# Optimization experiments

Measured on AMD Instinct MI355X. Metric: run time of the kernel, lower is better.

The kernel has to match this reference:

```python
import jax, jax.numpy as jnp
import numpy as np

B, T, D = 32, 4096, 64
K = 512
COMMITMENT_COST = 0.25


def setup_inputs() -> dict:
    key = jax.random.key(0)
    kz, kw = jax.random.split(key)
    z = jax.random.normal(kz, (B, T, D), dtype=jnp.float32)
    # matches nn.init.uniform_(weight, -1/K, 1/K)
    W = jax.random.uniform(kw, (K, D), dtype=jnp.float32, minval=-1.0 / K, maxval=1.0 / K)
    return {"z": z, "W": W}


def reference(z, W):
    b, t, d = z.shape
    z_flat = z.reshape(-1, d)                                   # [N, D]
    # squared euclidean distances via ||z||^2 + ||w||^2 - 2 z.w
    dist = (jnp.sum(z_flat * z_flat, axis=1, keepdims=True)
            + jnp.sum(W * W, axis=1)
            - 2.0 * z_flat @ W.T)                               # [N, K]
    indices = jnp.argmin(dist, axis=1)                          # [N]
    z_q = W[indices].reshape(b, t, d)                           # gather
    # straight-through estimator
    z_q_st = z + jax.lax.stop_gradient(z_q - z)
    loss = COMMITMENT_COST * jnp.mean((z - jax.lax.stop_gradient(z_q_st)) ** 2)
    return z_q_st, indices.reshape(b, t), loss
```

## Files before the change

### kernel.cpp

```cpp
#include <hip/hip_runtime.h>
#include <hip/hip_bf16.h>
#include <math.h>

#define NROWS 131072
#define KC    512
#define DD    64
#define NELEM (NROWS * DD)

#define OUT_IDX_OFF  NELEM
#define OUT_LOSS_OFF (NELEM + NROWS)

#define MARGIN 3e-5f

#define WSO_CNT   0
#define WSO_DONE  4
#define WSO_LOSS  8
#define WSO_WNORM 64
#define WSO_BH    4096
#define WSO_BL    (WSO_BH + 65536)
#define WSO_LIST  (WSO_BL + 65536)

typedef __attribute__((ext_vector_type(8))) short short8;
typedef __attribute__((ext_vector_type(4))) float f32x4;

__device__ __forceinline__ short f2bf_bits(float f) {
  __hip_bfloat16 h = __float2bfloat16(f);
  short s; __builtin_memcpy(&s, &h, 2); return s;
}
__device__ __forceinline__ float bfbits2f(short s) {
  __hip_bfloat16 h; __builtin_memcpy(&h, &s, 2);
  return __bfloat162float(h);
}
__device__ __forceinline__ void cvt8(const float* __restrict__ p, short8& hi, short8& lo) {
#pragma unroll
  for (int j = 0; j < 8; j++) {
    float f = p[j];
    short hb = f2bf_bits(f);
    float r = f - bfbits2f(hb);
    hi[j] = hb;
    lo[j] = f2bf_bits(r);
  }
}

__device__ __forceinline__ float np_sumsq64(const float* __restrict__ p) {
#pragma clang fp contract(off)
  float r0 = p[0] * p[0], r1 = p[1] * p[1], r2 = p[2] * p[2], r3 = p[3] * p[3];
  float r4 = p[4] * p[4], r5 = p[5] * p[5], r6 = p[6] * p[6], r7 = p[7] * p[7];
  for (int i = 8; i < 64; i += 8) {
    r0 = r0 + p[i + 0] * p[i + 0];
    r1 = r1 + p[i + 1] * p[i + 1];
    r2 = r2 + p[i + 2] * p[i + 2];
    r3 = r3 + p[i + 3] * p[i + 3];
    r4 = r4 + p[i + 4] * p[i + 4];
    r5 = r5 + p[i + 5] * p[i + 5];
    r6 = r6 + p[i + 6] * p[i + 6];
    r7 = r7 + p[i + 7] * p[i + 7];
  }
  return ((r0 + r1) + (r2 + r3)) + ((r4 + r5) + (r6 + r7));
}

__global__ void k_prep(const float* __restrict__ W, short8* __restrict__ Bh,
                       short8* __restrict__ Bl, float* __restrict__ wnorm,
                       int* __restrict__ flagCnt, int* __restrict__ doneCnt,
                       float* __restrict__ lossSum) {
  int gtid = blockIdx.x * blockDim.x + threadIdx.x;
  if (gtid == 0) { *flagCnt = 0; *doneCnt = 0; *lossSum = 0.0f; }
  int t = gtid >> 7, rem = gtid & 127;
  int h = rem >> 6, L = rem & 63;
  int cw = (t << 4) + (L & 15);
  int dbase = (h << 5) + ((L >> 4) << 3);
  short8 hi, lo;
  cvt8(W + (cw << 6) + dbase, hi, lo);
  Bh[gtid] = hi;
  Bl[gtid] = lo;
  if (gtid < KC) wnorm[gtid] = np_sumsq64(W + (gtid << 6));
}

__global__ void k_prep_z(const float* __restrict__ z, short8* __restrict__ Af) {
  int gtid = blockIdx.x * blockDim.x + threadIdx.x;
  int r16 = gtid >> 7, rem = gtid & 127;
  int h = rem >> 6, L = rem & 63;
  const float* zp = z + ((size_t)((r16 << 4) + (L & 15)) << 6) + (h << 5) + ((L >> 4) << 3);
  short8 hi, lo;
  cvt8(zp, hi, lo);
  size_t F = ((size_t)(r16 << 1) + h) << 1;
  Af[F * 64 + L] = hi;
  Af[(F + 1) * 64 + L] = lo;
}

#define MT 2
#define ROWS_PER_WAVE 32
#define ROWS_PER_BLOCK 256
#define SCREEN_THREADS 512

__global__ __launch_bounds__(SCREEN_THREADS, 4) void k_screen(
    const float* __restrict__ z, const float* __restrict__ W,
    const short8* __restrict__ Bh, const short8* __restrict__ Bl,
    const float* __restrict__ wnorm, float* out,
    int* __restrict__ flagList, int* __restrict__ flagCnt,
    float* __restrict__ lossSum) {
  const int tid = threadIdx.x;
  const int lane = tid & 63;
  const int wave = tid >> 6;
  const int m = lane & 15, quad = lane >> 4;
  const int rowBase = blockIdx.x * ROWS_PER_BLOCK + wave * ROWS_PER_WAVE;
  const int r16base = rowBase >> 4;

  __shared__ short8 sB[4096];

  const short8* Af = (const short8*)out;
  short8 Ah[MT][2], Al[MT][2];
#pragma unroll
  for (int mt = 0; mt < MT; mt++)
#pragma unroll
    for (int h = 0; h < 2; h++) {
      const size_t F = ((size_t)((r16base + mt) << 1) + h) << 1;
      Ah[mt][h] = Af[F * 64 + lane];
      Al[mt][h] = Af[(F + 1) * 64 + lane];
    }

  float b1[MT][4], b2[MT][4];
  int bi[MT][4];
#pragma unroll
  for (int mt = 0; mt < MT; mt++)
#pragma unroll
    for (int r = 0; r < 4; r++) { b1[mt][r] = 1e30f; b2[mt][r] = 1e30f; bi[mt][r] = 0; }

  for (int ph = 0; ph < 2; ph++) {
    if (ph) __syncthreads();
#pragma unroll
    for (int c = 0; c < 4; c++) {
      const int i = (c << 9) + tid;
      sB[i] = Bh[(ph << 11) + i];
      sB[2048 + i] = Bl[(ph << 11) + i];
    }
    __syncthreads();

#pragma unroll 2
    for (int tl = 0; tl < 16; tl++) {
      const int t = (ph << 4) + tl;
      short8 Bhf[2], Blf[2];
#pragma unroll
      for (int h = 0; h < 2; h++) {
        Bhf[h] = sB[(((tl << 1) + h) << 6) + lane];
        Blf[h] = sB[2048 + (((tl << 1) + h) << 6) + lane];
      }
      const float wn = wnorm[(t << 4) + m];

      f32x4 acc[MT] = {{0.f, 0.f, 0.f, 0.f}, {0.f, 0.f, 0.f, 0.f}};
#pragma unroll
      for (int h = 0; h < 2; h++) {
#pragma unroll
        for (int mt = 0; mt < MT; mt++)
          acc[mt] = __builtin_amdgcn_mfma_f32_16x16x32_bf16(Ah[mt][h], Bhf[h], acc[mt], 0, 0, 0);
#pragma unroll
        for (int mt = 0; mt < MT; mt++)
          acc[mt] = __builtin_amdgcn_mfma_f32_16x16x32_bf16(Al[mt][h], Bhf[h], acc[mt], 0, 0, 0);
#pragma unroll
        for (int mt = 0; mt < MT; mt++)
          acc[mt] = __builtin_amdgcn_mfma_f32_16x16x32_bf16(Ah[mt][h], Blf[h], acc[mt], 0, 0, 0);
      }

      const int colv = (t << 4) + m;
#pragma unroll
      for (int mt = 0; mt < MT; mt++)
#pragma unroll
        for (int r = 0; r < 4; r++) {
          float s = fmaf(-2.0f, acc[mt][r], wn);
          if (s < b1[mt][r]) { b2[mt][r] = b1[mt][r]; b1[mt][r] = s; bi[mt][r] = colv; }
          else b2[mt][r] = fminf(b2[mt][r], s);
        }
    }
  }

#pragma unroll
  for (int off = 1; off < 16; off <<= 1) {
#pragma unroll
    for (int mt = 0; mt < MT; mt++)
#pragma unroll
      for (int r = 0; r < 4; r++) {
        float o1 = __shfl_xor(b1[mt][r], off, 64);
        float o2 = __shfl_xor(b2[mt][r], off, 64);
        int oi = __shfl_xor(bi[mt][r], off, 64);
        if (o1 < b1[mt][r] || (o1 == b1[mt][r] && oi < bi[mt][r])) {
          b2[mt][r] = fminf(b1[mt][r], o2);
          b1[mt][r] = o1; bi[mt][r] = oi;
        } else {
          b2[mt][r] = fminf(b2[mt][r], o1);
        }
      }
  }

  float lossAcc = 0.f;
#pragma unroll
  for (int mt = 0; mt < MT; mt++)
#pragma unroll
    for (int r = 0; r < 4; r++) {
      const int row = rowBase + (mt << 4) + (quad << 2) + r;
      const int ki = bi[mt][r];
      f32x4 zv = *(const f32x4*)(z + (size_t)row * DD + (m << 2));
      f32x4 wv = *(const f32x4*)(W + (ki << 6) + (m << 2));
      f32x4 ov;
#pragma unroll
      for (int j = 0; j < 4; j++) {
        float tt = wv[j] - zv[j];
        ov[j] = zv[j] + tt;
        float dl = zv[j] - ov[j];
        lossAcc = fmaf(dl, dl, lossAcc);
      }
      *(f32x4*)(out + (size_t)row * DD + (m << 2)) = ov;
      if (m == 0) {
        out[OUT_IDX_OFF + row] = (float)ki;
        if (b2[mt][r] - b1[mt][r] < MARGIN) {
          int slot = atomicAdd(flagCnt, 1);
          flagList[slot] = row;
        }
      }
    }

#pragma unroll
  for (int off = 1; off < 64; off <<= 1) lossAcc += __shfl_xor(lossAcc, off, 64);
  if (lane == 0) atomicAdd(lossSum, lossAcc);
}

__global__ void k_refine(const float* __restrict__ z, const float* __restrict__ W,
                         const float* __restrict__ wnp, float* __restrict__ out,
                         const int* __restrict__ flagList,
                         const int* __restrict__ flagCnt,
                         float* __restrict__ lossSum, int* __restrict__ doneCnt) {
  int nflag = *flagCnt;
  int lane = threadIdx.x & 63;
  int wave = (blockIdx.x * blockDim.x + threadIdx.x) >> 6;
  int nWaves = (gridDim.x * blockDim.x) >> 6;

  for (int f = wave; f < nflag; f += nWaves) {
    int row = flagList[f];
    const float* zr = z + (size_t)row * DD;
    float A = np_sumsq64(zr);

    float best = 1e30f;
    int bk = 0x7fffffff;
#pragma unroll
    for (int j = 0; j < KC / 64; j++) {
      int k = lane + (j << 6);
      const float* wk = W + (k << 6);
      double cd = 0.0;
      for (int d = 0; d < DD; d++) cd = fma((double)zr[d], (double)wk[d], cd);
      float twoC = (float)(2.0 * cd);
      float dist;
      {
#pragma clang fp contract(off)
        float t1 = A + wnp[k];
        dist = t1 - twoC;
      }
      if (dist < best || (dist == best && k < bk)) { best = dist; bk = k; }
    }
#pragma unroll
    for (int off = 1; off < 64; off <<= 1) {
      float ov = __shfl_xor(best, off, 64);
      int ok = __shfl_xor(bk, off, 64);
      if (ov < best || (ov == best && ok < bk)) { best = ov; bk = ok; }
    }

    int kold = (int)out[OUT_IDX_OFF + row];
    if (bk != kold) {
      float zv = zr[lane];
      float wN = W[(bk << 6) + lane];
      float oOld = out[(size_t)row * DD + lane];
      float tN = wN - zv;
      float oN = zv + tN;
      out[(size_t)row * DD + lane] = oN;
      float dN = zv - oN, dO = zv - oOld;
      float delta = dN * dN - dO * dO;
#pragma unroll
      for (int off = 1; off < 64; off <<= 1) delta += __shfl_xor(delta, off, 64);
      if (lane == 0) {
        atomicAdd(lossSum, delta);
        out[OUT_IDX_OFF + row] = (float)bk;
      }
    }
  }

  __syncthreads();
  if (threadIdx.x == 0) {
    __threadfence();
    int d = atomicAdd(doneCnt, 1);
    if (d == (int)gridDim.x - 1) {
      float s = atomicAdd(lossSum, 0.0f);
      out[OUT_LOSS_OFF] = 0.25f * s / (float)NELEM;
    }
  }
}

extern "C" void kernel_launch(void* const* d_in, const int* in_sizes, int n_in,
                              void* d_out, int out_size, void* d_ws, size_t ws_size,
                              hipStream_t stream) {
  const float* z = (const float*)d_in[0];
  const float* W = (const float*)d_in[1];
  float* out = (float*)d_out;
  char* ws = (char*)d_ws;

  int* flagCnt = (int*)(ws + WSO_CNT);
  int* doneCnt = (int*)(ws + WSO_DONE);
  float* lossSum = (float*)(ws + WSO_LOSS);
  float* wnorm = (float*)(ws + WSO_WNORM);
  short8* Bh = (short8*)(ws + WSO_BH);
  short8* Bl = (short8*)(ws + WSO_BL);
  int* flagList = (int*)(ws + WSO_LIST);

  k_prep<<<16, 256, 0, stream>>>(W, Bh, Bl, wnorm, flagCnt, doneCnt, lossSum);
  k_prep_z<<<4096, 256, 0, stream>>>(z, (short8*)out);
  k_screen<<<NROWS / ROWS_PER_BLOCK, SCREEN_THREADS, 0, stream>>>(
      z, W, Bh, Bl, wnorm, out, flagList, flagCnt, lossSum);
  k_refine<<<256, 256, 0, stream>>>(z, W, wnorm, out, flagList, flagCnt,
                                    lossSum, doneCnt);
}
```

Baseline: 203.2 us.

## Fuse z bf16 split into screen kernel and pack argmin index into score bits

Removes the separate k_prep_z pass, which wrote a bf16 hi/lo copy of z to global memory. The screen kernel now converts z to hi/lo bf16 fragments directly in registers. The top-2 tracking uses unsigned keys that pack the codeword index into the low 9 mantissa bits of a positive-shifted score (wnorm+2), which turns the compare/select and the shuffle reduction into branchless unsigned min/max. Blocks shrink to 256 threads with 4 codebook phases and fully unrolled tiles, and the refine margin is widened to cover the precision lost to truncation, so more rows may be flagged for refinement.

```diff
diff --git a/kernel.cpp b/kernel.cpp
--- a/kernel.cpp
+++ b/kernel.cpp
@@ -10,7 +10,7 @@
 #define OUT_IDX_OFF  NELEM
 #define OUT_LOSS_OFF (NELEM + NROWS)
 
-#define MARGIN 3e-5f
+#define MARGIN_P 3.5e-4f
 
 #define WSO_CNT   0
 #define WSO_DONE  4
@@ -40,6 +40,13 @@
     hi[j] = hb;
     lo[j] = f2bf_bits(r);
   }
+}
+
+__device__ __forceinline__ unsigned f_as_u(float f) {
+  unsigned u; __builtin_memcpy(&u, &f, 4); return u;
+}
+__device__ __forceinline__ float u_as_f(unsigned u) {
+  float f; __builtin_memcpy(&f, &u, 4); return f;
 }
 
 __device__ __forceinline__ float np_sumsq64(const float* __restrict__ p) {
@@ -76,27 +83,17 @@
   if (gtid < KC) wnorm[gtid] = np_sumsq64(W + (gtid << 6));
 }
 
-__global__ void k_prep_z(const float* __restrict__ z, short8* __restrict__ Af) {
-  int gtid = blockIdx.x * blockDim.x + threadIdx.x;
-  int r16 = gtid >> 7, rem = gtid & 127;
-  int h = rem >> 6, L = rem & 63;
-  const float* zp = z + ((size_t)((r16 << 4) + (L & 15)) << 6) + (h << 5) + ((L >> 4) << 3);
-  short8 hi, lo;
-  cvt8(zp, hi, lo);
-  size_t F = ((size_t)(r16 << 1) + h) << 1;
-  Af[F * 64 + L] = hi;
-  Af[(F + 1) * 64 + L] = lo;
-}
-
 #define MT 2
 #define ROWS_PER_WAVE 32
-#define ROWS_PER_BLOCK 256
-#define SCREEN_THREADS 512
+#define ROWS_PER_BLOCK 128
+#define SCREEN_THREADS 256
+#define NPHASE 4
+#define TPP 8
 
 __global__ __launch_bounds__(SCREEN_THREADS, 4) void k_screen(
     const float* __restrict__ z, const float* __restrict__ W,
     const short8* __restrict__ Bh, const short8* __restrict__ Bl,
-    const float* __restrict__ wnorm, float* out,
+    const float* __restrict__ wnorm, float* __restrict__ out,
     int* __restrict__ flagList, int* __restrict__ flagCnt,
     float* __restrict__ lossSum) {
   const int tid = threadIdx.x;
@@ -104,48 +101,46 @@
   const int wave = tid >> 6;
   const int m = lane & 15, quad = lane >> 4;
   const int rowBase = blockIdx.x * ROWS_PER_BLOCK + wave * ROWS_PER_WAVE;
-  const int r16base = rowBase >> 4;
-
-  __shared__ short8 sB[4096];
-
-  const short8* Af = (const short8*)out;
+
+  __shared__ short8 sB[2048];
+
   short8 Ah[MT][2], Al[MT][2];
 #pragma unroll
+  for (int mt = 0; mt < MT; mt++) {
+    const float* zp = z + (size_t)(rowBase + (mt << 4) + m) * DD + (quad << 3);
+#pragma unroll
+    for (int h = 0; h < 2; h++) cvt8(zp + (h << 5), Ah[mt][h], Al[mt][h]);
+  }
+
+  unsigned b1[MT][4], b2[MT][4];
+#pragma unroll
   for (int mt = 0; mt < MT; mt++)
 #pragma unroll
-    for (int h = 0; h < 2; h++) {
-      const size_t F = ((size_t)((r16base + mt) << 1) + h) << 1;
-      Ah[mt][h] = Af[F * 64 + lane];
-      Al[mt][h] = Af[(F + 1) * 64 + lane];
-    }
-
-  float b1[MT][4], b2[MT][4];
-  int bi[MT][4];
-#pragma unroll
-  for (int mt = 0; mt < MT; mt++)
-#pragma unroll
-    for (int r = 0; r < 4; r++) { b1[mt][r] = 1e30f; b2[mt][r] = 1e30f; bi[mt][r] = 0; }
-
-  for (int ph = 0; ph < 2; ph++) {
+    for (int r = 0; r < 4; r++) { b1[mt][r] = 0xFFFFFFFFu; b2[mt][r] = 0xFFFFFFFFu; }
+
+  for (int ph = 0; ph < NPHASE; ph++) {
     if (ph) __syncthreads();
 #pragma unroll
     for (int c = 0; c < 4; c++) {
-      const int i = (c << 9) + tid;
-      sB[i] = Bh[(ph << 11) + i];
-      sB[2048 + i] = Bl[(ph << 11) + i];
+      const int i = (c << 8) + tid;
+      sB[i] = Bh[(ph << 10) + i];
+      sB[1024 + i] = Bl[(ph << 10) + i];
     }
     __syncthreads();
 
-#pragma unroll 2
-    for (int tl = 0; tl < 16; tl++) {
-      const int t = (ph << 4) + tl;
+    float wn2[TPP];
+#pragma unroll
+    for (int tl = 0; tl < TPP; tl++)
+      wn2[tl] = wnorm[((((ph << 3) + tl) << 4)) + m] + 2.0f;
+
+#pragma unroll
+    for (int tl = 0; tl < TPP; tl++) {
       short8 Bhf[2], Blf[2];
 #pragma unroll
       for (int h = 0; h < 2; h++) {
         Bhf[h] = sB[(((tl << 1) + h) << 6) + lane];
-        Blf[h] = sB[2048 + (((tl << 1) + h) << 6) + lane];
-      }
-      const float wn = wnorm[(t << 4) + m];
+        Blf[h] = sB[1024 + (((tl << 1) + h) << 6) + lane];
+      }
 
       f32x4 acc[MT] = {{0.f, 0.f, 0.f, 0.f}, {0.f, 0.f, 0.f, 0.f}};
 #pragma unroll
@@ -161,14 +156,16 @@
           acc[mt] = __builtin_amdgcn_mfma_f32_16x16x32_bf16(Ah[mt][h], Blf[h], acc[mt], 0, 0, 0);
       }
 
-      const int colv = (t << 4) + m;
+      const unsigned kb = (unsigned)(((((ph << 3) + tl) << 4)) + m);
 #pragma unroll
       for (int mt = 0; mt < MT; mt++)
 #pragma unroll
         for (int r = 0; r < 4; r++) {
-          float s = fmaf(-2.0f, acc[mt][r], wn);
-          if (s < b1[mt][r]) { b2[mt][r] = b1[mt][r]; b1[mt][r] = s; bi[mt][r] = colv; }
-          else b2[mt][r] = fminf(b2[mt][r], s);
+          float sf = fmaf(-2.0f, acc[mt][r], wn2[tl]);
+          unsigned sp = (f_as_u(sf) & 0xFFFFFE00u) | kb;
+          unsigned mx = b1[mt][r] > sp ? b1[mt][r] : sp;
+          b2[mt][r] = b2[mt][r] < mx ? b2[mt][r] : mx;
+          b1[mt][r] = b1[mt][r] < sp ? b1[mt][r] : sp;
         }
     }
   }
@@ -179,15 +176,12 @@
     for (int mt = 0; mt < MT; mt++)
 #pragma unroll
       for (int r = 0; r < 4; r++) {
-        float o1 = __shfl_xor(b1[mt][r], off, 64);
-        float o2 = __shfl_xor(b2[mt][r], off, 64);
-        int oi = __shfl_xor(bi[mt][r], off, 64);
-        if (o1 < b1[mt][r] || (o1 == b1[mt][r] && oi < bi[mt][r])) {
-          b2[mt][r] = fminf(b1[mt][r], o2);
-          b1[mt][r] = o1; bi[mt][r] = oi;
-        } else {
-          b2[mt][r] = fminf(b2[mt][r], o1);
-        }
+        unsigned o1 = (unsigned)__shfl_xor((int)b1[mt][r], off, 64);
+        unsigned o2 = (unsigned)__shfl_xor((int)b2[mt][r], off, 64);
+        unsigned mx = b1[mt][r] > o1 ? b1[mt][r] : o1;
+        unsigned mn2 = b2[mt][r] < o2 ? b2[mt][r] : o2;
+        b2[mt][r] = mn2 < mx ? mn2 : mx;
+        b1[mt][r] = b1[mt][r] < o1 ? b1[mt][r] : o1;
       }
   }
 
@@ -197,7 +191,7 @@
 #pragma unroll
     for (int r = 0; r < 4; r++) {
       const int row = rowBase + (mt << 4) + (quad << 2) + r;
-      const int ki = bi[mt][r];
+      const int ki = (int)(b1[mt][r] & 511u);
       f32x4 zv = *(const f32x4*)(z + (size_t)row * DD + (m << 2));
       f32x4 wv = *(const f32x4*)(W + (ki << 6) + (m << 2));
       f32x4 ov;
@@ -211,7 +205,9 @@
       *(f32x4*)(out + (size_t)row * DD + (m << 2)) = ov;
       if (m == 0) {
         out[OUT_IDX_OFF + row] = (float)ki;
-        if (b2[mt][r] - b1[mt][r] < MARGIN) {
+        float f1 = u_as_f(b1[mt][r] & 0xFFFFFE00u);
+        float f2 = u_as_f(b2[mt][r] & 0xFFFFFE00u);
+        if (f2 - f1 < MARGIN_P) {
           int slot = atomicAdd(flagCnt, 1);
           flagList[slot] = row;
         }
@@ -309,7 +305,6 @@
   int* flagList = (int*)(ws + WSO_LIST);
 
   k_prep<<<16, 256, 0, stream>>>(W, Bh, Bl, wnorm, flagCnt, doneCnt, lossSum);
-  k_prep_z<<<4096, 256, 0, stream>>>(z, (short8*)out);
   k_screen<<<NROWS / ROWS_PER_BLOCK, SCREEN_THREADS, 0, stream>>>(
       z, W, Bh, Bl, wnorm, out, flagList, flagCnt, lossSum);
   k_refine<<<256, 256, 0, stream>>>(z, W, wnorm, out, flagList, flagCnt,
```

Result: slower. 401.4 us (+97.5%).
